# Performance work log

Hardware: AMD Instinct MI355X
Metric: run time of the kernel (lower is better)

The kernel has to match this reference:

```python
import jax, jax.numpy as jnp
import numpy as np


def _discretize(A, B, C, step):
    # Bilinear (Tustin) discretization, as in the source module.
    N = A.shape[0]
    I = jnp.eye(N, dtype=A.dtype)
    BL = jnp.linalg.inv(I - (step / 2.0) * A)
    Ab = BL @ (I + (step / 2.0) * A)
    Bb = (BL * step) @ B  # (N, 1)
    return Ab, Bb, C


def _k_conv(Ab, Bb, Cb, L):
    # K[l] = Cb @ Ab^l @ Bb, computed by a linear recurrence instead of
    # L explicit matrix powers (same math as the source's K_conv).
    def step(v, _):
        k = (Cb @ v)[0, 0]
        return Ab @ v, k

    _, K = jax.lax.scan(step, Bb, None, length=L)
    return K  # (L,)


def setup_inputs() -> dict:
    key = jax.random.key(0)
    k_u, k_a, k_b, k_c, k_s = jax.random.split(key, 5)
    N, L, BATCH = 64, 16384, 512
    u = jax.random.normal(k_u, (BATCH, L), dtype=jnp.float32)
    # lecun_normal inits: std = 1/sqrt(fan_in)
    A = jax.random.normal(k_a, (N, N), dtype=jnp.float32) / np.sqrt(N)
    B = jax.random.normal(k_b, (N, 1), dtype=jnp.float32)  # fan_in = 1
    C = jax.random.normal(k_c, (1, N), dtype=jnp.float32) / np.sqrt(N)
    D = jnp.ones((1,), dtype=jnp.float32)
    # log_step_initializer(dt_min=1e-3, dt_max=0.1)
    lo, hi = np.log(1e-3), np.log(0.1)
    log_step = (jax.random.uniform(k_s, (1,)) * (hi - lo) + lo).astype(jnp.float32)
    return {"u": u, "A": A, "B": B, "C": C, "D": D, "log_step": log_step}


def reference(u, A, B, C, D, log_step) -> jnp.ndarray:
    L = u.shape[-1]
    step = jnp.exp(log_step)  # (1,)
    Ab, Bb, Cb = _discretize(A, B, C, step)
    K = _k_conv(Ab, Bb, Cb, L)  # (L,)
    # FFT causal convolution: pad both signals to length 2L (as in source),
    # multiply in frequency domain, take first L samples.
    n = 2 * L
    ud = jnp.fft.rfft(u, n=n, axis=-1)          # (BATCH, L+1) complex
    Kd = jnp.fft.rfft(K, n=n)                   # (L+1,) complex, broadcast
    y = jnp.fft.irfft(ud * Kd, n=n, axis=-1)[..., :L]
    return y + D * u
```

## Files before the change

kernel.cpp:

```cpp
#include <hip/hip_runtime.h>
#include <cstddef>

typedef double f64x4 __attribute__((ext_vector_type(4)));
typedef float  f32x4 __attribute__((ext_vector_type(4)));
typedef short  bf16x8 __attribute__((ext_vector_type(8)));

static constexpr int RCN = 512 * 128;

static constexpr size_t WS_W  = 0;
static constexpr size_t WS_G  = 8192;
static constexpr size_t WS_MD = 32768;

__device__ __forceinline__ unsigned short f2bf(float f) {
  union { float f; unsigned u; } v; v.f = f;
  unsigned u = v.u + 0x7FFFu + ((v.u >> 16) & 1u);
  return (unsigned short)(u >> 16);
}

__device__ __forceinline__ double probeE(int i, int k) {
  return (double)(((i * 3 + k * 5) & 7) - 3);
}
__device__ __forceinline__ double probeF(int k, int j) {
  return (double)(((k * 7 + j * 2) & 7) - 4);
}

__device__ __forceinline__ bool probe_mfma_layout(int lr, int lq, int rowm[4], int* colm_out)
{
  f64x4 z; z[0] = 0.0; z[1] = 0.0; z[2] = 0.0; z[3] = 0.0;
  f64x4 p1 = __builtin_amdgcn_mfma_f64_16x16x4f64((double)lr, 1.0, z, 0, 0, 0);
  f64x4 p2 = __builtin_amdgcn_mfma_f64_16x16x4f64(1.0, (double)lr, z, 0, 0, 0);
  bool okl = true;
#pragma unroll
  for (int r = 0; r < 4; ++r) {
    int rr = (int)(p1[r] * 0.25 + 0.5);
    okl = okl && (p1[r] == 4.0 * (double)rr) && rr >= 0 && rr < 16;
    rowm[r] = rr & 15;
    okl = okl && (p2[r] == p2[0]);
  }
  int cc = (int)(p2[0] * 0.25 + 0.5);
  okl = okl && (p2[0] == 4.0 * (double)cc) && cc >= 0 && cc < 16;
  *colm_out = cc & 15;
  f64x4 d = __builtin_amdgcn_mfma_f64_16x16x4f64(probeE(lr, lq), probeF(lq, lr), z, 0, 0, 0);
#pragma unroll
  for (int r = 0; r < 4; ++r) {
    double ref = 0.0;
#pragma unroll
    for (int k = 0; k < 4; ++k) ref += probeE(rowm[r], k) * probeF(k, cc & 15);
    okl = okl && (d[r] == ref);
  }
  return __all(okl) != 0;
}

__device__ __forceinline__ void mmPP_mfma(const double* A, const double* B,
                                          const double* Cin, double* D,
                                          int wi, int wj, int lr, int lq,
                                          const int rowm[4], int colm)
{
  f64x4 acc;
  if (Cin) {
#pragma unroll
    for (int r = 0; r < 4; ++r)
      acc[r] = Cin[(wi * 16 + rowm[r]) * 65 + wj * 16 + colm];
  } else {
    acc[0] = 0.0; acc[1] = 0.0; acc[2] = 0.0; acc[3] = 0.0;
  }
#pragma unroll
  for (int kb = 0; kb < 16; ++kb) {
    double a = A[(wi * 16 + lr) * 65 + kb * 4 + lq];
    double b = B[(kb * 4 + lq) * 65 + wj * 16 + lr];
    acc = __builtin_amdgcn_mfma_f64_16x16x4f64(a, b, acc, 0, 0, 0);
  }
#pragma unroll
  for (int r = 0; r < 4; ++r)
    D[(wi * 16 + rowm[r]) * 65 + wj * 16 + colm] = acc[r];
}

__device__ __forceinline__ void mmPP_valu(const double* A, const double* B,
                                          const double* Cin, double* D,
                                          int tr2, int tc2)
{
  double a00, a01, a10, a11;
  if (Cin) {
    a00 = Cin[(tr2 + 0) * 65 + tc2 + 0]; a01 = Cin[(tr2 + 0) * 65 + tc2 + 1];
    a10 = Cin[(tr2 + 1) * 65 + tc2 + 0]; a11 = Cin[(tr2 + 1) * 65 + tc2 + 1];
  } else { a00 = a01 = a10 = a11 = 0.0; }
#pragma unroll 8
  for (int c = 0; c < 64; ++c) {
    double av0 = A[(tr2 + 0) * 65 + c];
    double av1 = A[(tr2 + 1) * 65 + c];
    double bv0 = B[c * 65 + tc2 + 0];
    double bv1 = B[c * 65 + tc2 + 1];
    a00 = fma(av0, bv0, a00); a01 = fma(av0, bv1, a01);
    a10 = fma(av1, bv0, a10); a11 = fma(av1, bv1, a11);
  }
  D[(tr2 + 0) * 65 + tc2 + 0] = a00;
  D[(tr2 + 0) * 65 + tc2 + 1] = a01;
  D[(tr2 + 1) * 65 + tc2 + 0] = a10;
  D[(tr2 + 1) * 65 + tc2 + 1] = a11;
}

__device__ __forceinline__ void wh_tile(const float* Wf, const float* Hf,
                                        const double* Pd, float* Wo, float* Ho,
                                        int n, bool isW, int wi, int wj,
                                        int lr, int lq, const int rowm[4], int colm)
{
  f64x4 acc;
  acc[0] = 0.0; acc[1] = 0.0; acc[2] = 0.0; acc[3] = 0.0;
#pragma unroll
  for (int kb = 0; kb < 16; ++kb) {
    double a, b;
    if (isW) {
      a = (double)Wf[(wi * 16 + lr) * 65 + kb * 4 + lq];
      b = Pd[(wj * 16 + lr) * 65 + kb * 4 + lq];
    } else {
      a = (double)Hf[(wi * 16 + lr) * 65 + kb * 4 + lq];
      b = Pd[(kb * 4 + lq) * 65 + wj * 16 + lr];
    }
    acc = __builtin_amdgcn_mfma_f64_16x16x4f64(a, b, acc, 0, 0, 0);
  }
#pragma unroll
  for (int r = 0; r < 4; ++r) {
    int drow = wi * 16 + rowm[r];
    if (drow < n) {
      if (isW) Wo[(n + drow) * 65 + wj * 16 + colm] = (float)acc[r];
      else     Ho[(n + drow) * 65 + wj * 16 + colm] = (float)acc[r];
    }
  }
}

__global__ __launch_bounds__(1024) void k_precomp(
    const float* __restrict__ Ain, const float* __restrict__ Bin,
    const float* __restrict__ Cin, const float* __restrict__ Din,
    const float* __restrict__ LS, float* ws)
{
  __shared__ double SB0[64 * 65];
  __shared__ double SB1[64 * 65];
  __shared__ double SB2[64 * 65];
  __shared__ double SB3[64 * 65];
  __shared__ float  Kf[128];
  float* Wf = (float*)SB0;
  float* Hf = (float*)SB1;

  const int t    = threadIdx.x;
  const int wave = t >> 6;
  const int lane = t & 63;
  const int lr   = lane & 15;
  const int lq   = lane >> 4;
  const int wv_i = wave >> 2;
  const int wv_j = wave & 3;
  const int tr2  = (t >> 5) << 1;
  const int tc2  = (t & 31) << 1;

  int rowm[4]; int colm;
  const bool use_mfma = probe_mfma_layout(lr, lq, rowm, &colm);

  unsigned short* Wtg = (unsigned short*)(ws + WS_W);
  unsigned short* Gtg = (unsigned short*)(ws + WS_G);
  float* Mf = ws + WS_MD;

  const double step = exp((double)LS[0]);
  const double h = 0.5 * step;

  for (int idx = t; idx < 4096; idx += 1024) {
    int i = idx >> 6, j = idx & 63;
    double a = h * (double)Ain[idx];
    SB0[i * 65 + j] = a;
    SB2[i * 65 + j] = a + ((i == j) ? 1.0 : 0.0);
  }
  __syncthreads();

  {
    double *Xc = SB0, *Xn = SB1, *Zc = SB2, *Zn = SB3;
    for (int k = 0; k < 3; ++k) {
      if (use_mfma) mmPP_mfma(Xc, Xc, nullptr, Xn, wv_i, wv_j, lr, lq, rowm, colm);
      else          mmPP_valu(Xc, Xc, nullptr, Xn, tr2, tc2);
      __syncthreads();
      if (use_mfma) mmPP_mfma(Zc, Xn, Zc, Zn, wv_i, wv_j, lr, lq, rowm, colm);
      else          mmPP_valu(Zc, Xn, Zc, Zn, tr2, tc2);
      __syncthreads();
      double* tp_;
      tp_ = Xc; Xc = Xn; Xn = tp_;
      tp_ = Zc; Zc = Zn; Zn = tp_;
    }
  }

  if (t < 64) {
    double bb = 0.0;
    for (int c = 0; c < 64; ++c) bb = fma(SB3[t * 65 + c], (double)Bin[c], bb);
    Wf[t] = (float)(bb * step);
  }
  for (int idx = t; idx < 4096; idx += 1024) {
    int i = idx >> 6, j = idx & 63;
    SB2[i * 65 + j] = 2.0 * SB3[i * 65 + j] - ((i == j) ? 1.0 : 0.0);
  }
  __syncthreads();

  if (t < 64) {
    double hh = 0.0;
    for (int c = 0; c < 64; ++c) hh = fma((double)Cin[c], SB2[c * 65 + t], hh);
    Hf[t] = (float)hh;
  }
  __syncthreads();

  double* Pc = SB2;
  double* Pn = SB3;
  for (int k = 0; k < 7; ++k) {
    const int n = 1 << k;
    if (use_mfma) {
      const int tpm   = (n + 15) >> 4;
      const int tiles = tpm << 2;
      if (tiles <= 8) {
        if (wave < 2 * tiles) {
          const bool isW = wave < tiles;
          const int  wq  = isW ? wave : wave - tiles;
          wh_tile(Wf, Hf, Pc, Wf, Hf, n, isW, wq >> 2, wq & 3, lr, lq, rowm, colm);
        }
      } else {
        wh_tile(Wf, Hf, Pc, Wf, Hf, n, true,  wv_i, wv_j, lr, lq, rowm, colm);
        wh_tile(Wf, Hf, Pc, Wf, Hf, n, false, wv_i, wv_j, lr, lq, rowm, colm);
      }
      mmPP_mfma(Pc, Pc, nullptr, Pn, wv_i, wv_j, lr, lq, rowm, colm);
    } else {
      for (int o = t; o < (n << 6); o += 1024) {
        int r = o >> 6, ii = o & 63;
        double aw = 0.0, ah = 0.0;
#pragma unroll 4
        for (int c = 0; c < 64; ++c) {
          aw = fma(Pc[ii * 65 + c], (double)Wf[r * 65 + c], aw);
          ah = fma((double)Hf[r * 65 + c], Pc[c * 65 + ii], ah);
        }
        Wf[(n + r) * 65 + ii] = (float)aw;
        Hf[(n + r) * 65 + ii] = (float)ah;
      }
      mmPP_valu(Pc, Pc, nullptr, Pn, tr2, tc2);
    }
    __syncthreads();
    double* tp_ = Pc; Pc = Pn; Pn = tp_;
  }

  for (int idx = t; idx < 4096; idx += 1024) {
    int row = idx >> 6, col = idx & 63;
    Mf[((col >> 2) << 8) + (row << 2) + (col & 3)] = (float)Pc[row * 65 + col];
  }
  if (use_mfma) mmPP_mfma(Pc, Pc, nullptr, Pn, wv_i, wv_j, lr, lq, rowm, colm);
  else          mmPP_valu(Pc, Pc, nullptr, Pn, tr2, tc2);
  __syncthreads();
  for (int idx = t; idx < 4096; idx += 1024) {
    int row = idx >> 6, col = idx & 63;
    Mf[4096 + ((col >> 2) << 8) + (row << 2) + (col & 3)] = (float)Pn[row * 65 + col];
  }

  if (t < 128) {
    double s = 0.0;
    for (int c = 0; c < 64; ++c) s = fma((double)Cin[c], (double)Wf[t * 65 + c], s);
    Kf[t] = (float)s;
  }
  __syncthreads();

  for (int idx = t; idx < 8192; idx += 1024) {
    int i = idx >> 7, kk = idx & 127;
    Wtg[idx] = f2bf(Wf[(127 - kk) * 65 + i]);
  }
  const float Dval = Din[0];
  for (int idx = t; idx < 16384; idx += 1024) {
    int r = idx >> 7, kg = idx & 127;
    float v = (r >= kg) ? Kf[r - kg] : 0.f;
    if (kg == r) v += Dval;
    Gtg[r * 192 + kg] = f2bf(v);
  }
  for (int idx = t; idx < 8192; idx += 1024) {
    int r = idx >> 6, i = idx & 63;
    Gtg[r * 192 + 128 + i] = f2bf(Hf[r * 65 + i]);
  }
}

__global__ __launch_bounds__(256, 2) void k_fused(
    const float* __restrict__ u, const unsigned short* __restrict__ Wt,
    const unsigned short* __restrict__ Gt, const float* __restrict__ Mf,
    float* __restrict__ out)
{
  __shared__ __align__(16) unsigned char Lds[78848];
  float*          bs  = (float*)(Lds);
  unsigned short* WtS = (unsigned short*)(Lds + 34816);
  float*          dsb = (float*)(Lds + 34816);
  unsigned short* Gs  = (unsigned short*)(Lds);
  unsigned short* As  = (unsigned short*)(Lds + 52224);
  float*          xs  = (float*)(Lds + 62464);
  unsigned short* Xbf = (unsigned short*)(Lds + 62464);

  const int t    = threadIdx.x;
  const int w    = t >> 6;
  const int lane = t & 63;
  const int lr   = lane & 15, lq = lane >> 4;
  const int row  = blockIdx.x;
  const float* urow = u + ((size_t)row << 14);
  float* orow = out + ((size_t)row << 14);

  float Mr[64];
#pragma unroll
  for (int c4 = 0; c4 < 16; ++c4)
    *(float4*)&Mr[c4 * 4] = *(const float4*)&Mf[(c4 << 8) + (lane << 2)];

  auto stageA = [&](int k0) {
    for (int it = t; it < 1024; it += 256) {
      int rcl = it >> 3, k4 = (it & 7) << 2;
      float4 v = *(const float4*)&urow[(rcl << 7) + k0 + k4];
      ushort4 s;
      s.x = f2bf(v.x); s.y = f2bf(v.y); s.z = f2bf(v.z); s.w = f2bf(v.w);
      *(ushort4*)&As[rcl * 40 + k4] = s;
    }
  };

  {
    const unsigned* srcW = (const unsigned*)Wt;
    unsigned* dstW = (unsigned*)WtS;
    for (int idx = t; idx < 4096; idx += 256) {
      int r = idx >> 6, c = idx & 63;
      dstW[r * 68 + c] = srcW[idx];
    }
    stageA(0);
    __syncthreads();

    f32x4 acc[2][4];
#pragma unroll
    for (int i = 0; i < 2; ++i)
#pragma unroll
      for (int j = 0; j < 4; ++j) { acc[i][j][0] = 0.f; acc[i][j][1] = 0.f; acc[i][j][2] = 0.f; acc[i][j][3] = 0.f; }

    for (int sl = 0; sl < 4; ++sl) {
      bf16x8 av[2], bv[4];
#pragma unroll
      for (int ti = 0; ti < 2; ++ti)
        av[ti] = *(const bf16x8*)&As[(w * 32 + ti * 16 + lr) * 40 + lq * 8];
#pragma unroll
      for (int tj = 0; tj < 4; ++tj)
        bv[tj] = *(const bf16x8*)&WtS[(tj * 16 + lr) * 136 + sl * 32 + lq * 8];
#pragma unroll
      for (int ti = 0; ti < 2; ++ti)
#pragma unroll
        for (int tj = 0; tj < 4; ++tj)
          acc[ti][tj] = __builtin_amdgcn_mfma_f32_16x16x32_bf16(av[ti], bv[tj], acc[ti][tj], 0, 0, 0);
      if (sl < 3) {
        __syncthreads();
        stageA((sl + 1) << 5);
        __syncthreads();
      }
    }
#pragma unroll
    for (int ti = 0; ti < 2; ++ti)
#pragma unroll
      for (int tj = 0; tj < 4; ++tj)
#pragma unroll
        for (int r = 0; r < 4; ++r)
          bs[(w * 32 + ti * 16 + lq * 4 + r) * 68 + tj * 16 + lr] = acc[ti][tj][r];
    __syncthreads();
  }

  {
    stageA(0);

    for (int k = 0; k < 16; ++k) {
      const int tp = (w << 4) + k;
      float y0 = 0.f, y1 = 0.f, y2 = 0.f, y3 = 0.f;
#pragma unroll
      for (int c4 = 0; c4 < 16; ++c4) {
        float4 bb = *(const float4*)&bs[(tp << 1) * 68 + (c4 << 2)];
        y0 = fmaf(Mr[c4 * 4 + 0], bb.x, y0);
        y1 = fmaf(Mr[c4 * 4 + 1], bb.y, y1);
        y2 = fmaf(Mr[c4 * 4 + 2], bb.z, y2);
        y3 = fmaf(Mr[c4 * 4 + 3], bb.w, y3);
      }
      dsb[tp * 68 + lane] = ((y0 + y1) + (y2 + y3)) + bs[((tp << 1) + 1) * 68 + lane];
    }
    __syncthreads();

    if (w == 0) {
      float M2r[64];
#pragma unroll
      for (int c4 = 0; c4 < 16; ++c4)
        *(float4*)&M2r[c4 * 4] = *(const float4*)&Mf[4096 + (c4 << 8) + (lane << 2)];
      float x = 0.f;
      float ecur = dsb[lane];
      for (int u2 = 0; u2 < 64; ++u2) {
        xs[(u2 << 6) + lane] = x;
        float en = (u2 < 63) ? dsb[(u2 + 1) * 68 + lane] : 0.f;
        const unsigned xb = __float_as_uint(x);
        float y0 = 0.f, y1 = 0.f, y2 = 0.f, y3 = 0.f;
#pragma unroll
        for (int c = 0; c < 64; c += 4) {
          y0 = fmaf(M2r[c + 0], __uint_as_float(__builtin_amdgcn_readlane(xb, c + 0)), y0);
          y1 = fmaf(M2r[c + 1], __uint_as_float(__builtin_amdgcn_readlane(xb, c + 1)), y1);
          y2 = fmaf(M2r[c + 2], __uint_as_float(__builtin_amdgcn_readlane(xb, c + 2)), y2);
          y3 = fmaf(M2r[c + 3], __uint_as_float(__builtin_amdgcn_readlane(xb, c + 3)), y3);
        }
        x = ((y0 + y1) + (y2 + y3)) + ecur;
        ecur = en;
      }
    }
    __syncthreads();

    for (int k = 0; k < 16; ++k) {
      const int tp = (w << 4) + k;
      float y0 = 0.f, y1 = 0.f, y2 = 0.f, y3 = 0.f;
#pragma unroll
      for (int c4 = 0; c4 < 16; ++c4) {
        float4 xx = *(const float4*)&xs[(tp << 6) + (c4 << 2)];
        y0 = fmaf(Mr[c4 * 4 + 0], xx.x, y0);
        y1 = fmaf(Mr[c4 * 4 + 1], xx.y, y1);
        y2 = fmaf(Mr[c4 * 4 + 2], xx.z, y2);
        y3 = fmaf(Mr[c4 * 4 + 3], xx.w, y3);
      }
      float xeven = xs[(tp << 6) + lane];
      float xodd  = ((y0 + y1) + (y2 + y3)) + bs[(tp << 1) * 68 + lane];
      Xbf[((tp << 1) + 0) * 64 + lane] = f2bf(xeven);
      Xbf[((tp << 1) + 1) * 64 + lane] = f2bf(xodd);
    }
    __syncthreads();
  }

  {
    const unsigned* srcG = (const unsigned*)Gt;
    unsigned* dstG = (unsigned*)Gs;
    for (int idx = t; idx < 12288; idx += 256) {
      int r = idx / 96, c = idx - r * 96;
      dstG[r * 100 + c] = srcG[idx];
    }
    __syncthreads();

    f32x4 acc[2][8];
#pragma unroll
    for (int i = 0; i < 2; ++i)
#pragma unroll
      for (int j = 0; j < 8; ++j) { acc[i][j][0] = 0.f; acc[i][j][1] = 0.f; acc[i][j][2] = 0.f; acc[i][j][3] = 0.f; }

    for (int sl = 0; sl < 6; ++sl) {
      bf16x8 av[2], bv[8];
#pragma unroll
      for (int ti = 0; ti < 2; ++ti) {
        if (sl < 4)
          av[ti] = *(const bf16x8*)&As[(w * 32 + ti * 16 + lr) * 40 + lq * 8];
        else
          av[ti] = *(const bf16x8*)&Xbf[(w * 32 + ti * 16 + lr) * 64 + (sl - 4) * 32 + lq * 8];
      }
#pragma unroll
      for (int tj = 0; tj < 8; ++tj)
        bv[tj] = *(const bf16x8*)&Gs[(tj * 16 + lr) * 200 + sl * 32 + lq * 8];
#pragma unroll
      for (int ti = 0; ti < 2; ++ti)
#pragma unroll
        for (int tj = 0; tj < 8; ++tj)
          acc[ti][tj] = __builtin_amdgcn_mfma_f32_16x16x32_bf16(av[ti], bv[tj], acc[ti][tj], 0, 0, 0);
      if (sl < 3) {
        __syncthreads();
        stageA((sl + 1) << 5);
        __syncthreads();
      }
    }

#pragma unroll
    for (int ti = 0; ti < 2; ++ti)
#pragma unroll
      for (int tj = 0; tj < 8; ++tj)
#pragma unroll
        for (int r = 0; r < 4; ++r) {
          int rcl = w * 32 + ti * 16 + lq * 4 + r;
          orow[((size_t)rcl << 7) + tj * 16 + lr] = acc[ti][tj][r];
        }
  }
}

extern "C" void kernel_launch(void* const* d_in, const int* in_sizes, int n_in,
                              void* d_out, int out_size, void* d_ws, size_t ws_size,
                              hipStream_t stream) {
  (void)in_sizes; (void)n_in; (void)out_size; (void)ws_size;
  const float* u  = (const float*)d_in[0];
  const float* A  = (const float*)d_in[1];
  const float* Bv = (const float*)d_in[2];
  const float* Cv = (const float*)d_in[3];
  const float* Dv = (const float*)d_in[4];
  const float* ls = (const float*)d_in[5];
  float* out = (float*)d_out;
  float* ws  = (float*)d_ws;

  k_precomp<<<1, 1024, 0, stream>>>(A, Bv, Cv, Dv, ls, ws);
  k_fused<<<512, 256, 0, stream>>>(u, (const unsigned short*)(ws + WS_W),
                                   (const unsigned short*)(ws + WS_G),
                                   ws + WS_MD, out);
}
```

Measured before the change: 186.5 us.

## Prefetch global loads into registers ahead of LDS staging and split MFMA chains

The main per-row kernel now issues the global loads for the next u slice, the Wt weights and the Gt matrix into registers early, and writes them to LDS only after the current MFMA work or the serial recurrence. This hides global-memory latency behind compute, in particular overlapping the Gt load with the wave-0 scan. The precompute kernel's f64 MFMA loops are also split into two independent accumulators to break the dependency chain. The cost is much higher register pressure (64 extra registers for gv, plus nv and uv), which could lower occupancy or cause spills.

New measurement: 178.6 us. -4.3%, faster.

```diff
diff --git a/kernel.cpp b/kernel.cpp
--- a/kernel.cpp
+++ b/kernel.cpp
@@ -56,23 +56,27 @@
                                           int wi, int wj, int lr, int lq,
                                           const int rowm[4], int colm)
 {
-  f64x4 acc;
+  f64x4 a0, a1;
   if (Cin) {
 #pragma unroll
     for (int r = 0; r < 4; ++r)
-      acc[r] = Cin[(wi * 16 + rowm[r]) * 65 + wj * 16 + colm];
+      a0[r] = Cin[(wi * 16 + rowm[r]) * 65 + wj * 16 + colm];
   } else {
-    acc[0] = 0.0; acc[1] = 0.0; acc[2] = 0.0; acc[3] = 0.0;
-  }
-#pragma unroll
-  for (int kb = 0; kb < 16; ++kb) {
+    a0[0] = 0.0; a0[1] = 0.0; a0[2] = 0.0; a0[3] = 0.0;
+  }
+  a1[0] = 0.0; a1[1] = 0.0; a1[2] = 0.0; a1[3] = 0.0;
+#pragma unroll
+  for (int kb = 0; kb < 8; ++kb) {
     double a = A[(wi * 16 + lr) * 65 + kb * 4 + lq];
     double b = B[(kb * 4 + lq) * 65 + wj * 16 + lr];
-    acc = __builtin_amdgcn_mfma_f64_16x16x4f64(a, b, acc, 0, 0, 0);
+    a0 = __builtin_amdgcn_mfma_f64_16x16x4f64(a, b, a0, 0, 0, 0);
+    double a2 = A[(wi * 16 + lr) * 65 + (kb + 8) * 4 + lq];
+    double b2 = B[((kb + 8) * 4 + lq) * 65 + wj * 16 + lr];
+    a1 = __builtin_amdgcn_mfma_f64_16x16x4f64(a2, b2, a1, 0, 0, 0);
   }
 #pragma unroll
   for (int r = 0; r < 4; ++r)
-    D[(wi * 16 + rowm[r]) * 65 + wj * 16 + colm] = acc[r];
+    D[(wi * 16 + rowm[r]) * 65 + wj * 16 + colm] = a0[r] + a1[r];
 }
 
 __device__ __forceinline__ void mmPP_valu(const double* A, const double* B,
@@ -104,26 +108,33 @@
                                         int n, bool isW, int wi, int wj,
                                         int lr, int lq, const int rowm[4], int colm)
 {
-  f64x4 acc;
-  acc[0] = 0.0; acc[1] = 0.0; acc[2] = 0.0; acc[3] = 0.0;
-#pragma unroll
-  for (int kb = 0; kb < 16; ++kb) {
-    double a, b;
+  f64x4 a0, a1;
+  a0[0] = 0.0; a0[1] = 0.0; a0[2] = 0.0; a0[3] = 0.0;
+  a1[0] = 0.0; a1[1] = 0.0; a1[2] = 0.0; a1[3] = 0.0;
+#pragma unroll
+  for (int kb = 0; kb < 8; ++kb) {
+    double a, b, a2, b2;
     if (isW) {
-      a = (double)Wf[(wi * 16 + lr) * 65 + kb * 4 + lq];
-      b = Pd[(wj * 16 + lr) * 65 + kb * 4 + lq];
+      a  = (double)Wf[(wi * 16 + lr) * 65 + kb * 4 + lq];
+      b  = Pd[(wj * 16 + lr) * 65 + kb * 4 + lq];
+      a2 = (double)Wf[(wi * 16 + lr) * 65 + (kb + 8) * 4 + lq];
+      b2 = Pd[(wj * 16 + lr) * 65 + (kb + 8) * 4 + lq];
     } else {
-      a = (double)Hf[(wi * 16 + lr) * 65 + kb * 4 + lq];
-      b = Pd[(kb * 4 + lq) * 65 + wj * 16 + lr];
-    }
-    acc = __builtin_amdgcn_mfma_f64_16x16x4f64(a, b, acc, 0, 0, 0);
+      a  = (double)Hf[(wi * 16 + lr) * 65 + kb * 4 + lq];
+      b  = Pd[(kb * 4 + lq) * 65 + wj * 16 + lr];
+      a2 = (double)Hf[(wi * 16 + lr) * 65 + (kb + 8) * 4 + lq];
+      b2 = Pd[((kb + 8) * 4 + lq) * 65 + wj * 16 + lr];
+    }
+    a0 = __builtin_amdgcn_mfma_f64_16x16x4f64(a,  b,  a0, 0, 0, 0);
+    a1 = __builtin_amdgcn_mfma_f64_16x16x4f64(a2, b2, a1, 0, 0, 0);
   }
 #pragma unroll
   for (int r = 0; r < 4; ++r) {
     int drow = wi * 16 + rowm[r];
     if (drow < n) {
-      if (isW) Wo[(n + drow) * 65 + wj * 16 + colm] = (float)acc[r];
-      else     Ho[(n + drow) * 65 + wj * 16 + colm] = (float)acc[r];
+      float v = (float)(a0[r] + a1[r]);
+      if (isW) Wo[(n + drow) * 65 + wj * 16 + colm] = v;
+      else     Ho[(n + drow) * 65 + wj * 16 + colm] = v;
     }
   }
 }
@@ -296,31 +307,40 @@
   const float* urow = u + ((size_t)row << 14);
   float* orow = out + ((size_t)row << 14);
 
+  unsigned wtv[16];
+#pragma unroll
+  for (int j = 0; j < 16; ++j) wtv[j] = ((const unsigned*)Wt)[t + j * 256];
+  float4 uv[4];
+#pragma unroll
+  for (int j = 0; j < 4; ++j) {
+    int it = t + j * 256;
+    int rcl = it >> 3, k4 = (it & 7) << 2;
+    uv[j] = *(const float4*)&urow[(rcl << 7) + k4];
+  }
   float Mr[64];
 #pragma unroll
   for (int c4 = 0; c4 < 16; ++c4)
     *(float4*)&Mr[c4 * 4] = *(const float4*)&Mf[(c4 << 8) + (lane << 2)];
 
-  auto stageA = [&](int k0) {
-    for (int it = t; it < 1024; it += 256) {
-      int rcl = it >> 3, k4 = (it & 7) << 2;
-      float4 v = *(const float4*)&urow[(rcl << 7) + k0 + k4];
-      ushort4 s;
-      s.x = f2bf(v.x); s.y = f2bf(v.y); s.z = f2bf(v.z); s.w = f2bf(v.w);
-      *(ushort4*)&As[rcl * 40 + k4] = s;
-    }
-  };
-
   {
-    const unsigned* srcW = (const unsigned*)Wt;
     unsigned* dstW = (unsigned*)WtS;
-    for (int idx = t; idx < 4096; idx += 256) {
-      int r = idx >> 6, c = idx & 63;
-      dstW[r * 68 + c] = srcW[idx];
-    }
-    stageA(0);
-    __syncthreads();
-
+#pragma unroll
+    for (int j = 0; j < 16; ++j) {
+      int idx = t + j * 256;
+      dstW[(idx >> 6) * 68 + (idx & 63)] = wtv[j];
+    }
+  }
+#pragma unroll
+  for (int j = 0; j < 4; ++j) {
+    int it = t + j * 256;
+    int rcl = it >> 3, k4 = (it & 7) << 2;
+    ushort4 s;
+    s.x = f2bf(uv[j].x); s.y = f2bf(uv[j].y); s.z = f2bf(uv[j].z); s.w = f2bf(uv[j].w);
+    *(ushort4*)&As[rcl * 40 + k4] = s;
+  }
+  __syncthreads();
+
+  {
     f32x4 acc[2][4];
 #pragma unroll
     for (int i = 0; i < 2; ++i)
@@ -328,6 +348,15 @@
       for (int j = 0; j < 4; ++j) { acc[i][j][0] = 0.f; acc[i][j][1] = 0.f; acc[i][j][2] = 0.f; acc[i][j][3] = 0.f; }
 
     for (int sl = 0; sl < 4; ++sl) {
+      float4 nv[4];
+      if (sl < 3) {
+#pragma unroll
+        for (int j = 0; j < 4; ++j) {
+          int it = t + j * 256;
+          int rcl = it >> 3, k4 = (it & 7) << 2;
+          nv[j] = *(const float4*)&urow[(rcl << 7) + ((sl + 1) << 5) + k4];
+        }
+      }
       bf16x8 av[2], bv[4];
 #pragma unroll
       for (int ti = 0; ti < 2; ++ti)
@@ -342,7 +371,14 @@
           acc[ti][tj] = __builtin_amdgcn_mfma_f32_16x16x32_bf16(av[ti], bv[tj], acc[ti][tj], 0, 0, 0);
       if (sl < 3) {
         __syncthreads();
-        stageA((sl + 1) << 5);
+#pragma unroll
+        for (int j = 0; j < 4; ++j) {
+          int it = t + j * 256;
+          int rcl = it >> 3, k4 = (it & 7) << 2;
+          ushort4 s;
+          s.x = f2bf(nv[j].x); s.y = f2bf(nv[j].y); s.z = f2bf(nv[j].z); s.w = f2bf(nv[j].w);
+          *(ushort4*)&As[rcl * 40 + k4] = s;
+        }
         __syncthreads();
       }
     }
@@ -357,7 +393,13 @@
   }
 
   {
-    stageA(0);
+    float4 p3v[4];
+#pragma unroll
+    for (int j = 0; j < 4; ++j) {
+      int it = t + j * 256;
+      int rcl = it >> 3, k4 = (it & 7) << 2;
+      p3v[j] = *(const float4*)&urow[(rcl << 7) + k4];
+    }
 
     for (int k = 0; k < 16; ++k) {
       const int tp = (w << 4) + k;
@@ -372,7 +414,23 @@
       }
       dsb[tp * 68 + lane] = ((y0 + y1) + (y2 + y3)) + bs[((tp << 1) + 1) * 68 + lane];
     }
+#pragma unroll
+    for (int j = 0; j < 4; ++j) {
+      int it = t + j * 256;
+      int rcl = it >> 3, k4 = (it & 7) << 2;
+      ushort4 s;
+      s.x = f2bf(p3v[j].x); s.y = f2bf(p3v[j].y); s.z = f2bf(p3v[j].z); s.w = f2bf(p3v[j].w);
+      *(ushort4*)&As[rcl * 40 + k4] = s;
+    }
     __syncthreads();
+
+    unsigned gv[64];
+    if (w > 0) {
+      const int t192 = t - 64;
+#pragma unroll
+      for (int j = 0; j < 64; ++j)
+        gv[j] = ((const unsigned*)Gt)[j * 192 + t192];
+    }
 
     if (w == 0) {
       float M2r[64];
@@ -416,17 +474,20 @@
       Xbf[((tp << 1) + 1) * 64 + lane] = f2bf(xodd);
     }
     __syncthreads();
+
+    if (w > 0) {
+      const int t192 = t - 64;
+      const int hi = (t192 >= 96) ? 1 : 0;
+      const int lo = t192 - 96 * hi;
+      unsigned* dstG = (unsigned*)Gs;
+#pragma unroll
+      for (int j = 0; j < 64; ++j)
+        dstG[(2 * j + hi) * 100 + lo] = gv[j];
+    }
+    __syncthreads();
   }
 
   {
-    const unsigned* srcG = (const unsigned*)Gt;
-    unsigned* dstG = (unsigned*)Gs;
-    for (int idx = t; idx < 12288; idx += 256) {
-      int r = idx / 96, c = idx - r * 96;
-      dstG[r * 100 + c] = srcG[idx];
-    }
-    __syncthreads();
-
     f32x4 acc[2][8];
 #pragma unroll
     for (int i = 0; i < 2; ++i)
@@ -434,6 +495,15 @@
       for (int j = 0; j < 8; ++j) { acc[i][j][0] = 0.f; acc[i][j][1] = 0.f; acc[i][j][2] = 0.f; acc[i][j][3] = 0.f; }
 
     for (int sl = 0; sl < 6; ++sl) {
+      float4 nv[4];
+      if (sl < 3) {
+#pragma unroll
+        for (int j = 0; j < 4; ++j) {
+          int it = t + j * 256;
+          int rcl = it >> 3, k4 = (it & 7) << 2;
+          nv[j] = *(const float4*)&urow[(rcl << 7) + ((sl + 1) << 5) + k4];
+        }
+      }
       bf16x8 av[2], bv[8];
 #pragma unroll
       for (int ti = 0; ti < 2; ++ti) {
@@ -452,7 +522,14 @@
           acc[ti][tj] = __builtin_amdgcn_mfma_f32_16x16x32_bf16(av[ti], bv[tj], acc[ti][tj], 0, 0, 0);
       if (sl < 3) {
         __syncthreads();
-        stageA((sl + 1) << 5);
+#pragma unroll
+        for (int j = 0; j < 4; ++j) {
+          int it = t + j * 256;
+          int rcl = it >> 3, k4 = (it & 7) << 2;
+          ushort4 s;
+          s.x = f2bf(nv[j].x); s.y = f2bf(nv[j].y); s.z = f2bf(nv[j].z); s.w = f2bf(nv[j].w);
+          *(ushort4*)&As[rcl * 40 + k4] = s;
+        }
         __syncthreads();
       }
     }
```
